# Kernel optimization log

Measured on AMD Instinct MI355X. Metric: run time of the kernel, lower is better.

Reference implementation:

```python
import jax, jax.numpy as jnp
import numpy as np

B, S, D = 2, 2048, 1024
H, DH = 16, 64
NEG = -1e9


def setup_inputs() -> dict:
    key = jax.random.key(0)
    ks = jax.random.split(key, 4)
    hidden_states = jax.random.normal(ks[0], (B, S, D), dtype=jnp.float32)
    # additive causal mask: 0 where allowed, -1e9 where masked
    causal = jnp.tril(jnp.ones((S, S), dtype=bool))
    attention_mask = jnp.where(causal, 0.0, NEG).astype(jnp.float32)[None, None]
    Wqkv = jax.random.normal(ks[1], (D, 3 * H * DH), dtype=jnp.float32) * (1.0 / np.sqrt(D))
    bqkv = jnp.zeros((3 * H * DH,), dtype=jnp.float32)
    Wproj = jax.random.normal(ks[2], (H * DH, D), dtype=jnp.float32) * (1.0 / np.sqrt(H * DH))
    bproj = jnp.zeros((D,), dtype=jnp.float32)
    return {"hidden_states": hidden_states, "attention_mask": attention_mask,
            "Wqkv": Wqkv, "bqkv": bqkv, "Wproj": Wproj, "bproj": bproj}


def reference(hidden_states, attention_mask, Wqkv, bqkv, Wproj, bproj):
    b, s, _ = hidden_states.shape
    scale = 1.0 / np.sqrt(DH)
    qkv = hidden_states @ Wqkv + bqkv                      # [b, s, 3*H*DH]
    q, k, v = jnp.split(qkv, 3, axis=-1)
    # [b, s, H*DH] -> [b, H, s, DH]
    def split_heads(x):
        return x.reshape(b, s, H, DH).transpose(0, 2, 1, 3)
    q, k, v = split_heads(q), split_heads(k), split_heads(v)
    scores = jnp.einsum('bhqd,bhkd->bhqk', q, k) * scale   # [b, H, s, s]
    scores = scores + attention_mask
    probs = jax.nn.softmax(scores, axis=-1)
    attn = jnp.einsum('bhqk,bhkd->bhqd', probs, v)         # [b, H, s, DH]
    attn = attn.transpose(0, 2, 1, 3).reshape(b, s, H * DH)
    out = attn @ Wproj + bproj                             # [b, s, D]
    return out
```

## Files before the change

### kernel.cpp

```cpp
#include <hip/hip_runtime.h>
#include <hip/hip_bf16.h>
#include <stdint.h>

#define B_ 2
#define S_ 2048
#define D_ 1024
#define H_ 16
#define DH_ 64
#define M_ 4096
#define LOG2E 1.44269504088896340736f

typedef __attribute__((ext_vector_type(8))) short short8;
typedef __attribute__((ext_vector_type(4))) float f32x4;
typedef __attribute__((ext_vector_type(16))) float f32x16;

__device__ __forceinline__ unsigned short f2bf(float f) {
  __hip_bfloat16 h = __float2bfloat16(f);
  union { __hip_bfloat16 h; unsigned short u; } cv;
  cv.h = h;
  return cv.u;
}

__device__ __forceinline__ unsigned int pack_bf(float lo, float hi2) {
  union { __hip_bfloat162 h; unsigned int u; } cv;
  cv.h = __float22bfloat162_rn(make_float2(lo, hi2));
  return cv.u;
}

__device__ __forceinline__ void gll16(const void* g, void* l) {
  __builtin_amdgcn_global_load_lds(
      (__attribute__((address_space(1))) void*)(g),
      (__attribute__((address_space(3))) void*)(l), 16, 0, 0);
}

__global__ __launch_bounds__(256) void k_prep(const float* __restrict__ hs,
                                              const float* __restrict__ Wqkv,
                                              const float* __restrict__ Wproj,
                                              unsigned short* __restrict__ hid,
                                              unsigned short* __restrict__ wqkvT,
                                              unsigned short* __restrict__ wprT) {
  __shared__ unsigned short tile[32][33];
  const int id = blockIdx.x;
  if (id < 4096) {
    const int i = id * 256 + threadIdx.x;
    float4 v = reinterpret_cast<const float4*>(hs)[i];
    ushort4 o;
    o.x = f2bf(v.x); o.y = f2bf(v.y); o.z = f2bf(v.z); o.w = f2bf(v.w);
    reinterpret_cast<ushort4*>(hid)[i] = o;
    return;
  }
  const float* W;
  unsigned short* WT;
  int N, i;
  if (id < 7168) { i = id - 4096; W = Wqkv; WT = wqkvT; N = 3072; }
  else           { i = id - 7168; W = Wproj; WT = wprT; N = 1024; }
  const int nb = (N == 3072) ? 96 : 32;
  const int n0 = (i % nb) * 32, k0 = (i / nb) * 32;
  const int tx = threadIdx.x & 31, ty = threadIdx.x >> 5;
#pragma unroll
  for (int j = 0; j < 4; j++) {
    int k = ty + j * 8;
    tile[k][tx] = f2bf(W[(long)(k0 + k) * N + n0 + tx]);
  }
  __syncthreads();
#pragma unroll
  for (int j = 0; j < 4; j++) {
    int n = ty + j * 8;
    WT[(long)(n0 + n) * 1024 + k0 + tx] = tile[tx][n];
  }
}

template <int MODE, int BN>
__global__ __launch_bounds__(256) void k_gemm(
    const unsigned short* __restrict__ A,
    const unsigned short* __restrict__ BT,
    const float* __restrict__ bias,
    void* __restrict__ out0,
    unsigned short* __restrict__ outk,
    unsigned short* __restrict__ outv,
    int M, int N, int K) {
  constexpr int JN = BN / 32;
  __shared__ __align__(16) unsigned short lds_a[128 * 32];
  __shared__ __align__(16) unsigned short lds_b[BN * 32];
  const int t = threadIdx.x;
  const int w = t >> 6, l = t & 63;
  const int g = l >> 4, x = l & 15;
  const int wr = w >> 1, wc = w & 1;
  const long m0 = (long)blockIdx.x * 128, n0 = (long)blockIdx.y * BN;

  f32x4 acc[4][JN];
#pragma unroll
  for (int i = 0; i < 4; i++)
#pragma unroll
    for (int j = 0; j < JN; j++) acc[i][j] = (f32x4){0.f, 0.f, 0.f, 0.f};

  const unsigned short* ga = A + (m0 + 16 * w + (l >> 2)) * (long)K + (l & 3) * 8;
  const unsigned short* gb = BT + (n0 + 16 * w + (l >> 2)) * (long)K + (l & 3) * 8;
  unsigned short* la = lds_a + w * 512;
  unsigned short* lb = lds_b + w * 512;

  for (int k0 = 0; k0 < K; k0 += 32) {
    __syncthreads();
    gll16(ga + k0, la);
    gll16(ga + k0 + 64 * (long)K, la + 2048);
    gll16(gb + k0, lb);
    if (BN == 128) gll16(gb + k0 + 64 * (long)K, lb + 2048);
    __syncthreads();
    short8 af[4], bfr[JN];
#pragma unroll
    for (int i = 0; i < 4; i++)
      af[i] = *reinterpret_cast<const short8*>(lds_a + (wr * 64 + i * 16 + x) * 32 + g * 8);
#pragma unroll
    for (int j = 0; j < JN; j++)
      bfr[j] = *reinterpret_cast<const short8*>(
          lds_b + (wc * (BN / 2) + j * 16 + x) * 32 + g * 8);
#pragma unroll
    for (int i = 0; i < 4; i++)
#pragma unroll
      for (int j = 0; j < JN; j++)
        acc[i][j] = __builtin_amdgcn_mfma_f32_16x16x32_bf16(af[i], bfr[j], acc[i][j], 0, 0, 0);
  }

#pragma unroll
  for (int i = 0; i < 4; i++) {
#pragma unroll
    for (int j = 0; j < JN; j++) {
#pragma unroll
      for (int r = 0; r < 4; r++) {
        const long m = m0 + wr * 64 + i * 16 + 4 * g + r;
        const long n = n0 + wc * (BN / 2) + j * 16 + x;
        float v = acc[i][j][r] + bias[n];
        if (MODE == 1) {
          ((float*)out0)[m * N + n] = v;
        } else {
          const int b = (int)(m >> 11), s = (int)(m & 2047);
          const int which = (int)(n >> 10);
          const int rem = (int)(n & 1023);
          const int h = rem >> 6, d = rem & 63;
          const long idx = (((long)(b * H_ + h)) * S_ + s) * DH_ + d;
          unsigned short bv = f2bf(v);
          if (which == 0) ((unsigned short*)out0)[idx] = bv;
          else if (which == 1) outk[idx] = bv;
          else outv[idx] = bv;
        }
      }
    }
  }
}

__global__ __launch_bounds__(256) void k_tr_v(const unsigned short* __restrict__ v,
                                              unsigned short* __restrict__ vt) {
  __shared__ __align__(16) unsigned short tile[64][72];
  const int bh = blockIdx.y;
  const int s0 = blockIdx.x * 64;
  const int t = threadIdx.x;
  const int r = t >> 2;
  const int c = (t & 3) * 16;
  const unsigned short* src = v + ((long)bh * S_ + s0 + r) * DH_ + c;
  *reinterpret_cast<short8*>(&tile[r][c]) = *reinterpret_cast<const short8*>(src);
  *reinterpret_cast<short8*>(&tile[r][c + 8]) = *reinterpret_cast<const short8*>(src + 8);
  __syncthreads();
  unsigned short* dst = vt + ((long)bh * DH_ + r) * S_ + s0 + c;
#pragma unroll
  for (int jj = 0; jj < 2; jj++) {
    short8 o;
#pragma unroll
    for (int j = 0; j < 8; j++) o[j] = (short)tile[c + jj * 8 + j][r];
    *reinterpret_cast<short8*>(dst + jj * 8) = o;
  }
}

__global__ __launch_bounds__(256, 1) void k_attn(const unsigned short* __restrict__ qb_,
                                                 const unsigned short* __restrict__ kb,
                                                 const unsigned short* __restrict__ vt,
                                                 unsigned short* __restrict__ attn_out) {
  __shared__ __align__(16) unsigned short lds_k[2][4096];
  __shared__ __align__(16) unsigned short lds_v[2][4096];

  const int t0_ = threadIdx.x;
  const int w = t0_ >> 6, l = t0_ & 63;
  const int q32 = l & 31, hi = l >> 5;
  const int r7 = q32 & 7;
  const int lr = l >> 3, sch = (l & 7) ^ lr;

  const int id = blockIdx.x;
  const int xcd = id & 7, slot = id >> 3;
  const int bh = xcd + 8 * (slot >> 4);
  const int craw = slot & 15;
  const int qc = (slot & 32) ? craw : (15 - craw);

  const int b = bh >> 4, h = bh & 15;
  const long kvbase = (long)bh * S_ * DH_;
  const long vtbase = (long)bh * DH_ * S_;
  const float SC = 0.125f * LOG2E;

  const int q0p = qc * 128;
  const int q0w = q0p + 32 * w;
  const int qg = q0w + q32;
  const int nt = 2 * qc + 2;

  short8 qf[4];
#pragma unroll
  for (int f = 0; f < 4; f++)
    qf[f] = *reinterpret_cast<const short8*>(qb_ + kvbase + (long)qg * DH_ + 16 * f + 8 * hi);

#pragma unroll
  for (int i = 0; i < 2; i++) {
    gll16(kb + kvbase + (long)(16 * w + 8 * i + lr) * DH_ + sch * 8,
          &lds_k[0][w * 1024 + i * 512]);
    gll16(vt + vtbase + (long)(16 * w + 8 * i + lr) * S_ + sch * 8,
          &lds_v[0][w * 1024 + i * 512]);
  }

  f32x16 oacc[2];
#pragma unroll
  for (int dt = 0; dt < 2; dt++)
#pragma unroll
    for (int r = 0; r < 16; r++) oacc[dt][r] = 0.f;
  float m = -1.0e30f, lown = 0.f;

  asm volatile("s_waitcnt vmcnt(0)" ::: "memory");
  __syncthreads();

  for (int tt = 0; tt < nt; tt++) {
    const int kv0 = tt * 64;
    if (tt + 1 < nt) {
      const int nb = (tt + 1) & 1;
      const int kvn = kv0 + 64;
#pragma unroll
      for (int i = 0; i < 2; i++) {
        gll16(kb + kvbase + (long)(kvn + 16 * w + 8 * i + lr) * DH_ + sch * 8,
              &lds_k[nb][w * 1024 + i * 512]);
        gll16(vt + vtbase + (long)(16 * w + 8 * i + lr) * S_ + kvn + sch * 8,
              &lds_v[nb][w * 1024 + i * 512]);
      }
    }

    if (kv0 <= q0w + 31) {
      const unsigned short* lk = lds_k[tt & 1];
      const unsigned short* lv = lds_v[tt & 1];

      f32x16 sa[2];
#pragma unroll
      for (int ks = 0; ks < 2; ks++) {
#pragma unroll
        for (int r = 0; r < 16; r++) sa[ks][r] = 0.f;
#pragma unroll
        for (int f = 0; f < 4; f++) {
          short8 kf = *reinterpret_cast<const short8*>(
              lk + (32 * ks + q32) * 64 + (((2 * f + hi) ^ r7) << 3));
          sa[ks] = __builtin_amdgcn_mfma_f32_32x32x16_bf16(kf, qf[f], sa[ks], 0, 0, 0);
        }
      }

      float p[32];
#pragma unroll
      for (int ks = 0; ks < 2; ks++)
#pragma unroll
        for (int r = 0; r < 16; r++) p[16 * ks + r] = sa[ks][r] * SC;

      const bool diag = (kv0 + 63 > q0w);
      if (diag) {
#pragma unroll
        for (int ks = 0; ks < 2; ks++)
#pragma unroll
          for (int r = 0; r < 16; r++) {
            const int kvg = kv0 + 32 * ks + (r & 3) + 8 * (r >> 2) + 4 * hi;
            if (kvg > qg) p[16 * ks + r] = -1.0e30f;
          }
      }

      float mx[16];
#pragma unroll
      for (int r = 0; r < 16; r++) mx[r] = fmaxf(p[r], p[r + 16]);
#pragma unroll
      for (int st = 8; st >= 1; st >>= 1)
#pragma unroll
        for (int r = 0; r < 8; r++)
          if (r < st) mx[r] = fmaxf(mx[r], mx[r + st]);
      float pmax = fmaxf(mx[0], __shfl_xor(mx[0], 32, 64));

      if (__any(pmax > m + 8.0f)) {
        const float mn = fmaxf(m, pmax);
        const float fsc = exp2f(m - mn);
        m = mn;
        lown *= fsc;
#pragma unroll
        for (int r = 0; r < 16; r++) {
          const int rr = (r & 3) + 8 * (r >> 2) + 4 * hi;
          const float fr = __int_as_float(
              __builtin_amdgcn_ds_bpermute(rr << 2, __float_as_int(fsc)));
          oacc[0][r] *= fr;
          oacc[1][r] *= fr;
        }
      }

#pragma unroll
      for (int i = 0; i < 32; i++) p[i] = exp2f(p[i] - m);

      float sm[16];
#pragma unroll
      for (int r = 0; r < 16; r++) sm[r] = p[r] + p[r + 16];
#pragma unroll
      for (int st = 8; st >= 1; st >>= 1)
#pragma unroll
        for (int r = 0; r < 8; r++)
          if (r < st) sm[r] += sm[r + st];
      lown += sm[0];

#pragma unroll
      for (int s4 = 0; s4 < 4; s4++) {
        const int bse = 8 * s4;
        unsigned int t0p = pack_bf(p[bse + 0], p[bse + 1]);
        unsigned int t1p = pack_bf(p[bse + 2], p[bse + 3]);
        unsigned int t2p = pack_bf(p[bse + 4], p[bse + 5]);
        unsigned int t3p = pack_bf(p[bse + 6], p[bse + 7]);
        unsigned int s0 = hi ? t0p : t2p;
        unsigned int s1 = hi ? t1p : t3p;
        unsigned int x0 = __shfl_xor(s0, 32, 64);
        unsigned int x1 = __shfl_xor(s1, 32, 64);
        union { unsigned int u[4]; short8 s8; } pa;
        pa.u[0] = hi ? x0 : t0p;
        pa.u[1] = hi ? x1 : t1p;
        pa.u[2] = hi ? t2p : x0;
        pa.u[3] = hi ? t3p : x1;
#pragma unroll
        for (int dt = 0; dt < 2; dt++) {
          short8 vf = *reinterpret_cast<const short8*>(
              lv + (32 * dt + q32) * 64 + (((2 * s4 + hi) ^ r7) << 3));
          oacc[dt] = __builtin_amdgcn_mfma_f32_32x32x16_bf16(pa.s8, vf, oacc[dt], 0, 0, 0);
        }
      }
    }

    asm volatile("s_waitcnt vmcnt(0)" ::: "memory");
    __syncthreads();
  }

  const float lt = lown + __shfl_xor(lown, 32, 64);
  const float linv = 1.0f / lt;
#pragma unroll
  for (int r = 0; r < 16; r++) {
    const int rr = (r & 3) + 8 * (r >> 2) + 4 * hi;
    const float li = __int_as_float(
        __builtin_amdgcn_ds_bpermute(rr << 2, __float_as_int(linv)));
    const long row = (long)b * S_ + q0w + rr;
#pragma unroll
    for (int dt = 0; dt < 2; dt++)
      attn_out[row * (H_ * DH_) + h * DH_ + 32 * dt + q32] = f2bf(oacc[dt][r] * li);
  }
}

extern "C" void kernel_launch(void* const* d_in, const int* in_sizes, int n_in,
                              void* d_out, int out_size, void* d_ws, size_t ws_size,
                              hipStream_t stream) {
  (void)in_sizes; (void)n_in; (void)out_size; (void)ws_size;
  const float* hs    = (const float*)d_in[0];
  const float* Wqkv  = (const float*)d_in[2];
  const float* bqkv  = (const float*)d_in[3];
  const float* Wproj = (const float*)d_in[4];
  const float* bproj = (const float*)d_in[5];
  float* out = (float*)d_out;

  unsigned short* ws    = (unsigned short*)d_ws;
  unsigned short* hid   = ws;
  unsigned short* wqkvT = hid + 4194304;
  unsigned short* wprT  = wqkvT + 3145728;
  unsigned short* q_b   = wprT + 1048576;
  unsigned short* k_b   = q_b + 4194304;
  unsigned short* v_b   = k_b + 4194304;
  unsigned short* vt_b  = v_b + 4194304;
  unsigned short* ao    = vt_b + 4194304;

  k_prep<<<8192, 256, 0, stream>>>(hs, Wqkv, Wproj, hid, wqkvT, wprT);
  k_gemm<0, 128><<<dim3(32, 24), 256, 0, stream>>>(hid, wqkvT, bqkv, (void*)q_b, k_b, v_b,
                                                   4096, 3072, 1024);
  k_tr_v<<<dim3(32, 32), 256, 0, stream>>>(v_b, vt_b);
  k_attn<<<512, 256, 0, stream>>>(q_b, k_b, vt_b, ao);
  k_gemm<1, 64><<<dim3(32, 16), 256, 0, stream>>>(ao, wprT, bproj, (void*)out, nullptr, nullptr,
                                                  4096, 1024, 1024);
}
```

Measured before the change: 221.5 us.

## Double-buffer GEMM LDS tiles and widen attention KV tiles to 128

The GEMM kernel now uses two LDS buffers and prefetches the next K-slice while running MFMAs on the current one, replacing the old two-barrier-per-iteration load/compute sequence. The attention kernel processes 128 keys per iteration instead of 64, with a new V-tile swizzle, half as many loop trips and barriers, and the causal mask applied only on the last tile. The trade-off is doubled LDS use in both kernels and more registers per thread in attention (64 score values), which may lower occupancy. Warps whose rows lie below part of the diagonal tile now also compute fully masked score blocks.

```diff
diff --git a/kernel.cpp b/kernel.cpp
--- a/kernel.cpp
+++ b/kernel.cpp
@@ -80,8 +80,8 @@
     unsigned short* __restrict__ outv,
     int M, int N, int K) {
   constexpr int JN = BN / 32;
-  __shared__ __align__(16) unsigned short lds_a[128 * 32];
-  __shared__ __align__(16) unsigned short lds_b[BN * 32];
+  __shared__ __align__(16) unsigned short lds_a[2][128 * 32];
+  __shared__ __align__(16) unsigned short lds_b[2][BN * 32];
   const int t = threadIdx.x;
   const int w = t >> 6, l = t & 63;
   const int g = l >> 4, x = l & 15;
@@ -96,29 +96,40 @@
 
   const unsigned short* ga = A + (m0 + 16 * w + (l >> 2)) * (long)K + (l & 3) * 8;
   const unsigned short* gb = BT + (n0 + 16 * w + (l >> 2)) * (long)K + (l & 3) * 8;
-  unsigned short* la = lds_a + w * 512;
-  unsigned short* lb = lds_b + w * 512;
-
-  for (int k0 = 0; k0 < K; k0 += 32) {
-    __syncthreads();
+
+  auto stage = [&](int nb, int k0) {
+    unsigned short* la = lds_a[nb] + w * 512;
+    unsigned short* lb = lds_b[nb] + w * 512;
     gll16(ga + k0, la);
     gll16(ga + k0 + 64 * (long)K, la + 2048);
     gll16(gb + k0, lb);
     if (BN == 128) gll16(gb + k0 + 64 * (long)K, lb + 2048);
-    __syncthreads();
+  };
+
+  stage(0, 0);
+  asm volatile("s_waitcnt vmcnt(0)" ::: "memory");
+  __syncthreads();
+
+  const int nit = K >> 5;
+  for (int it = 0; it < nit; it++) {
+    const int cur = it & 1;
+    if (it + 1 < nit) stage(cur ^ 1, (it + 1) << 5);
     short8 af[4], bfr[JN];
 #pragma unroll
     for (int i = 0; i < 4; i++)
-      af[i] = *reinterpret_cast<const short8*>(lds_a + (wr * 64 + i * 16 + x) * 32 + g * 8);
+      af[i] = *reinterpret_cast<const short8*>(
+          lds_a[cur] + (wr * 64 + i * 16 + x) * 32 + g * 8);
 #pragma unroll
     for (int j = 0; j < JN; j++)
       bfr[j] = *reinterpret_cast<const short8*>(
-          lds_b + (wc * (BN / 2) + j * 16 + x) * 32 + g * 8);
+          lds_b[cur] + (wc * (BN / 2) + j * 16 + x) * 32 + g * 8);
 #pragma unroll
     for (int i = 0; i < 4; i++)
 #pragma unroll
       for (int j = 0; j < JN; j++)
         acc[i][j] = __builtin_amdgcn_mfma_f32_16x16x32_bf16(af[i], bfr[j], acc[i][j], 0, 0, 0);
+    asm volatile("s_waitcnt vmcnt(0)" ::: "memory");
+    __syncthreads();
   }
 
 #pragma unroll
@@ -174,14 +185,16 @@
                                                  const unsigned short* __restrict__ kb,
                                                  const unsigned short* __restrict__ vt,
                                                  unsigned short* __restrict__ attn_out) {
-  __shared__ __align__(16) unsigned short lds_k[2][4096];
-  __shared__ __align__(16) unsigned short lds_v[2][4096];
+  __shared__ __align__(16) unsigned short lds_k[2][8192];
+  __shared__ __align__(16) unsigned short lds_v[2][8192];
 
   const int t0_ = threadIdx.x;
   const int w = t0_ >> 6, l = t0_ & 63;
   const int q32 = l & 31, hi = l >> 5;
   const int r7 = q32 & 7;
+  const int r15 = q32 & 15;
   const int lr = l >> 3, sch = (l & 7) ^ lr;
+  const int lv4 = l >> 4;
 
   const int id = blockIdx.x;
   const int xcd = id & 7, slot = id >> 3;
@@ -194,23 +207,30 @@
   const long vtbase = (long)bh * DH_ * S_;
   const float SC = 0.125f * LOG2E;
 
-  const int q0p = qc * 128;
-  const int q0w = q0p + 32 * w;
+  const int q0w = qc * 128 + 32 * w;
   const int qg = q0w + q32;
-  const int nt = 2 * qc + 2;
+  const int nt = qc + 1;
+
+  const unsigned short* kbb = kb + kvbase;
+  const unsigned short* vtb = vt + vtbase;
+
+  auto stage = [&](int nb, int kv0) {
+#pragma unroll
+    for (int i = 0; i < 4; i++) {
+      const int R0 = 32 * w + 8 * i;
+      gll16(kbb + (long)(kv0 + R0 + lr) * 64 + sch * 8, &lds_k[nb][R0 * 64]);
+      const int V0 = 16 * w + 4 * i;
+      const int svch = (l & 15) ^ (4 * i + lv4);
+      gll16(vtb + (long)(V0 + lv4) * S_ + kv0 + svch * 8, &lds_v[nb][V0 * 128]);
+    }
+  };
 
   short8 qf[4];
 #pragma unroll
   for (int f = 0; f < 4; f++)
     qf[f] = *reinterpret_cast<const short8*>(qb_ + kvbase + (long)qg * DH_ + 16 * f + 8 * hi);
 
-#pragma unroll
-  for (int i = 0; i < 2; i++) {
-    gll16(kb + kvbase + (long)(16 * w + 8 * i + lr) * DH_ + sch * 8,
-          &lds_k[0][w * 1024 + i * 512]);
-    gll16(vt + vtbase + (long)(16 * w + 8 * i + lr) * S_ + sch * 8,
-          &lds_v[0][w * 1024 + i * 512]);
-  }
+  stage(0, 0);
 
   f32x16 oacc[2];
 #pragma unroll
@@ -223,113 +243,97 @@
   __syncthreads();
 
   for (int tt = 0; tt < nt; tt++) {
-    const int kv0 = tt * 64;
-    if (tt + 1 < nt) {
-      const int nb = (tt + 1) & 1;
-      const int kvn = kv0 + 64;
-#pragma unroll
-      for (int i = 0; i < 2; i++) {
-        gll16(kb + kvbase + (long)(kvn + 16 * w + 8 * i + lr) * DH_ + sch * 8,
-              &lds_k[nb][w * 1024 + i * 512]);
-        gll16(vt + vtbase + (long)(16 * w + 8 * i + lr) * S_ + kvn + sch * 8,
-              &lds_v[nb][w * 1024 + i * 512]);
-      }
-    }
-
-    if (kv0 <= q0w + 31) {
-      const unsigned short* lk = lds_k[tt & 1];
-      const unsigned short* lv = lds_v[tt & 1];
-
-      f32x16 sa[2];
-#pragma unroll
-      for (int ks = 0; ks < 2; ks++) {
-#pragma unroll
-        for (int r = 0; r < 16; r++) sa[ks][r] = 0.f;
-#pragma unroll
-        for (int f = 0; f < 4; f++) {
-          short8 kf = *reinterpret_cast<const short8*>(
-              lk + (32 * ks + q32) * 64 + (((2 * f + hi) ^ r7) << 3));
-          sa[ks] = __builtin_amdgcn_mfma_f32_32x32x16_bf16(kf, qf[f], sa[ks], 0, 0, 0);
+    const int kv0 = tt << 7;
+    if (tt + 1 < nt) stage((tt + 1) & 1, kv0 + 128);
+
+    const unsigned short* lk = lds_k[tt & 1];
+    const unsigned short* lv = lds_v[tt & 1];
+
+    float p[64];
+    const bool diag = (tt == nt - 1);
+#pragma unroll
+    for (int ks = 0; ks < 4; ks++) {
+      f32x16 sa;
+#pragma unroll
+      for (int r = 0; r < 16; r++) sa[r] = 0.f;
+#pragma unroll
+      for (int f = 0; f < 4; f++) {
+        short8 kf = *reinterpret_cast<const short8*>(
+            lk + (32 * ks + q32) * 64 + (((2 * f + hi) ^ r7) << 3));
+        sa = __builtin_amdgcn_mfma_f32_32x32x16_bf16(kf, qf[f], sa, 0, 0, 0);
+      }
+#pragma unroll
+      for (int r = 0; r < 16; r++) {
+        float s = sa[r] * SC;
+        if (diag) {
+          const int kvg = kv0 + 32 * ks + (r & 3) + 8 * (r >> 2) + 4 * hi;
+          if (kvg > qg) s = -1.0e30f;
         }
-      }
-
-      float p[32];
-#pragma unroll
-      for (int ks = 0; ks < 2; ks++)
-#pragma unroll
-        for (int r = 0; r < 16; r++) p[16 * ks + r] = sa[ks][r] * SC;
-
-      const bool diag = (kv0 + 63 > q0w);
-      if (diag) {
-#pragma unroll
-        for (int ks = 0; ks < 2; ks++)
-#pragma unroll
-          for (int r = 0; r < 16; r++) {
-            const int kvg = kv0 + 32 * ks + (r & 3) + 8 * (r >> 2) + 4 * hi;
-            if (kvg > qg) p[16 * ks + r] = -1.0e30f;
-          }
-      }
-
-      float mx[16];
-#pragma unroll
-      for (int r = 0; r < 16; r++) mx[r] = fmaxf(p[r], p[r + 16]);
-#pragma unroll
-      for (int st = 8; st >= 1; st >>= 1)
-#pragma unroll
-        for (int r = 0; r < 8; r++)
-          if (r < st) mx[r] = fmaxf(mx[r], mx[r + st]);
-      float pmax = fmaxf(mx[0], __shfl_xor(mx[0], 32, 64));
-
-      if (__any(pmax > m + 8.0f)) {
-        const float mn = fmaxf(m, pmax);
-        const float fsc = exp2f(m - mn);
-        m = mn;
-        lown *= fsc;
-#pragma unroll
-        for (int r = 0; r < 16; r++) {
-          const int rr = (r & 3) + 8 * (r >> 2) + 4 * hi;
-          const float fr = __int_as_float(
-              __builtin_amdgcn_ds_bpermute(rr << 2, __float_as_int(fsc)));
-          oacc[0][r] *= fr;
-          oacc[1][r] *= fr;
-        }
-      }
-
-#pragma unroll
-      for (int i = 0; i < 32; i++) p[i] = exp2f(p[i] - m);
-
-      float sm[16];
-#pragma unroll
-      for (int r = 0; r < 16; r++) sm[r] = p[r] + p[r + 16];
-#pragma unroll
-      for (int st = 8; st >= 1; st >>= 1)
-#pragma unroll
-        for (int r = 0; r < 8; r++)
-          if (r < st) sm[r] += sm[r + st];
-      lown += sm[0];
-
-#pragma unroll
-      for (int s4 = 0; s4 < 4; s4++) {
-        const int bse = 8 * s4;
-        unsigned int t0p = pack_bf(p[bse + 0], p[bse + 1]);
-        unsigned int t1p = pack_bf(p[bse + 2], p[bse + 3]);
-        unsigned int t2p = pack_bf(p[bse + 4], p[bse + 5]);
-        unsigned int t3p = pack_bf(p[bse + 6], p[bse + 7]);
-        unsigned int s0 = hi ? t0p : t2p;
-        unsigned int s1 = hi ? t1p : t3p;
-        unsigned int x0 = __shfl_xor(s0, 32, 64);
-        unsigned int x1 = __shfl_xor(s1, 32, 64);
-        union { unsigned int u[4]; short8 s8; } pa;
-        pa.u[0] = hi ? x0 : t0p;
-        pa.u[1] = hi ? x1 : t1p;
-        pa.u[2] = hi ? t2p : x0;
-        pa.u[3] = hi ? t3p : x1;
-#pragma unroll
-        for (int dt = 0; dt < 2; dt++) {
-          short8 vf = *reinterpret_cast<const short8*>(
-              lv + (32 * dt + q32) * 64 + (((2 * s4 + hi) ^ r7) << 3));
-          oacc[dt] = __builtin_amdgcn_mfma_f32_32x32x16_bf16(pa.s8, vf, oacc[dt], 0, 0, 0);
-        }
+        p[16 * ks + r] = s;
+      }
+    }
+
+    float mx[16];
+#pragma unroll
+    for (int r = 0; r < 16; r++)
+      mx[r] = fmaxf(fmaxf(p[r], p[r + 16]), fmaxf(p[r + 32], p[r + 48]));
+#pragma unroll
+    for (int st = 8; st >= 1; st >>= 1)
+#pragma unroll
+      for (int r = 0; r < 8; r++)
+        if (r < st) mx[r] = fmaxf(mx[r], mx[r + st]);
+    float pmax = fmaxf(mx[0], __shfl_xor(mx[0], 32, 64));
+
+    if (__any(pmax > m + 8.0f)) {
+      const float mn = fmaxf(m, pmax);
+      const float fsc = exp2f(m - mn);
+      m = mn;
+      lown *= fsc;
+#pragma unroll
+      for (int r = 0; r < 16; r++) {
+        const int rr = (r & 3) + 8 * (r >> 2) + 4 * hi;
+        const float fr = __int_as_float(
+            __builtin_amdgcn_ds_bpermute(rr << 2, __float_as_int(fsc)));
+        oacc[0][r] *= fr;
+        oacc[1][r] *= fr;
+      }
+    }
+
+#pragma unroll
+    for (int i = 0; i < 64; i++) p[i] = exp2f(p[i] - m);
+
+    float sm[16];
+#pragma unroll
+    for (int r = 0; r < 16; r++)
+      sm[r] = (p[r] + p[r + 16]) + (p[r + 32] + p[r + 48]);
+#pragma unroll
+    for (int st = 8; st >= 1; st >>= 1)
+#pragma unroll
+      for (int r = 0; r < 8; r++)
+        if (r < st) sm[r] += sm[r + st];
+    lown += sm[0];
+
+#pragma unroll
+    for (int s4 = 0; s4 < 8; s4++) {
+      const int bse = 8 * s4;
+      unsigned int t0p = pack_bf(p[bse + 0], p[bse + 1]);
+      unsigned int t1p = pack_bf(p[bse + 2], p[bse + 3]);
+      unsigned int t2p = pack_bf(p[bse + 4], p[bse + 5]);
+      unsigned int t3p = pack_bf(p[bse + 6], p[bse + 7]);
+      unsigned int s0 = hi ? t0p : t2p;
+      unsigned int s1 = hi ? t1p : t3p;
+      unsigned int x0 = __shfl_xor(s0, 32, 64);
+      unsigned int x1 = __shfl_xor(s1, 32, 64);
+      union { unsigned int u[4]; short8 s8; } pa;
+      pa.u[0] = hi ? x0 : t0p;
+      pa.u[1] = hi ? x1 : t1p;
+      pa.u[2] = hi ? t2p : x0;
+      pa.u[3] = hi ? t3p : x1;
+#pragma unroll
+      for (int dt = 0; dt < 2; dt++) {
+        short8 vf = *reinterpret_cast<const short8*>(
+            lv + (32 * dt + q32) * 128 + (((2 * s4 + hi) ^ r15) << 3));
+        oacc[dt] = __builtin_amdgcn_mfma_f32_32x32x16_bf16(pa.s8, vf, oacc[dt], 0, 0, 0);
       }
     }
 
```

After: 212.8 us. 3.9% less time.
